# Performance work log

Hardware: AMD Instinct MI355X
Metric: run time of the kernel (lower is better)

## Reference

```python
import jax, jax.numpy as jnp
import numpy as np

B, I, O = 1024, 512, 512
EPS = 1e-07
LOG_CLIP = 20.0

def setup_inputs() -> dict:
    key = jax.random.key(0)
    k1, k2, k3, k4 = jax.random.split(key, 4)
    x = jax.random.normal(k1, (B, I), dtype=jnp.float32)
    # match tf.random_normal_initializer(mean, stddev) used in the layer
    w_hat = 0.88 + 0.2 * jax.random.normal(k2, (I, O), dtype=jnp.float32)
    m_hat = 0.5 + 0.2 * jax.random.normal(k3, (I, O), dtype=jnp.float32)
    g = 0.2 * jax.random.normal(k4, (O,), dtype=jnp.float32)
    return {"x": x, "w_hat": w_hat, "m_hat": m_hat, "g": g}

def reference(x, w_hat, m_hat, g):
    w1 = jnp.tanh(w_hat) * jax.nn.sigmoid(m_hat)          # [I, O]
    a = x @ w1                                             # [B, O] additive path
    # multiplicative path: exp(log|x| @ w1), clipped at 20 before exp
    logx = jnp.log(jnp.maximum(jnp.abs(x), EPS))           # [B, I]
    m1 = jnp.exp(jnp.minimum(logx @ w1, LOG_CLIP))         # [B, O]
    # sign-product tracking. TF flattens w1 row-major to [I*O], tiles x
    # O times along axis 1 -> xs[b, k] = x[b, k % I]; so after reshape to
    # [B, O, I], the paired weight magnitude is ws[j, i] = |w1.flat[j*I + i]|.
    ws_oi = jnp.abs(w1.reshape(-1)).reshape(O, I)          # [O, I] (faithful to TF reshape)
    sgn_x = jnp.sign(x)                                    # [B, I]
    sgn = sgn_x[:, None, :] * ws_oi[None, :, :] + (1.0 - ws_oi)[None, :, :]  # [B, O, I]
    ms = jnp.prod(sgn, axis=2)                             # [B, O]
    g1 = jax.nn.sigmoid(g)                                 # [O]
    return g1 * a + (1.0 - g1) * m1 * jnp.clip(ms, -1.0, 1.0)
```

## Files before the change

### kernel.cpp

```cpp
#include <hip/hip_runtime.h>


#define O_N 512
#define I_N 512
#define B_N 1024

typedef _Float16 f16;
typedef _Float16 f16x8 __attribute__((ext_vector_type(8)));
typedef float f32x4 __attribute__((ext_vector_type(4)));

__device__ __forceinline__ float fast_sigmoid(float v) {
    return 1.0f / (1.0f + __expf(-v));
}
__device__ __forceinline__ float fast_tanh(float v) {
    return 1.0f - 2.0f / (1.0f + __expf(2.0f * v));
}

__global__ __launch_bounds__(256) void prep_kernel(const float* __restrict__ x,
                                                   const float* __restrict__ wh,
                                                   const float* __restrict__ mh,
                                                   f16x8* __restrict__ apx,
                                                   f16x8* __restrict__ apl,
                                                   f16x8* __restrict__ bp) {
    const int tid = threadIdx.x;
    if (blockIdx.x < 128) {
        __shared__ f16 lt[32][72];
        const int kb = blockIdx.x >> 3;
        const int nb = blockIdx.x & 7;
        const int r  = tid >> 3;
        const int c0 = (tid & 7) * 8;
        const int base = (kb * 32 + r) * O_N + nb * 64 + c0;
        const float4* w4 = (const float4*)(wh + base);
        const float4* m4 = (const float4*)(mh + base);
        const float4 wa = w4[0], wb = w4[1], ma = m4[0], mb = m4[1];
        f16x8 row;
        row[0] = (f16)(fast_tanh(wa.x) * fast_sigmoid(ma.x));
        row[1] = (f16)(fast_tanh(wa.y) * fast_sigmoid(ma.y));
        row[2] = (f16)(fast_tanh(wa.z) * fast_sigmoid(ma.z));
        row[3] = (f16)(fast_tanh(wa.w) * fast_sigmoid(ma.w));
        row[4] = (f16)(fast_tanh(wb.x) * fast_sigmoid(mb.x));
        row[5] = (f16)(fast_tanh(wb.y) * fast_sigmoid(mb.y));
        row[6] = (f16)(fast_tanh(wb.z) * fast_sigmoid(mb.z));
        row[7] = (f16)(fast_tanh(wb.w) * fast_sigmoid(mb.w));
        *(f16x8*)&lt[r][c0] = row;
        __syncthreads();
        const int fl  = tid & 63;
        const int tnl = tid >> 6;
        const int nl  = tnl * 16 + (fl & 15);
        const int k0  = (fl >> 4) * 8;
        f16x8 bf;
#pragma unroll
        for (int j = 0; j < 8; ++j) bf[j] = lt[k0 + j][nl];
        const int tn_g = nb * 4 + tnl;
        bp[tn_g * 1024 + kb * 64 + fl] = bf;
    } else {
        const int t  = (blockIdx.x - 128) * 256 + tid;
        const int fl = t & 63;
        const int tk = (t >> 6) & 15;
        const int tm = t >> 10;
        const int m  = tm * 16 + (fl & 15);
        const int k0 = tk * 32 + (fl >> 4) * 8;
        const float4* x4 = (const float4*)(x + m * I_N + k0);
        const float4 q0 = x4[0], q1 = x4[1];
        const float vx[8] = {q0.x, q0.y, q0.z, q0.w, q1.x, q1.y, q1.z, q1.w};
        f16x8 fx, fv;
#pragma unroll
        for (int j = 0; j < 8; ++j) {
            fx[j] = (f16)vx[j];
            fv[j] = (f16)__logf(fmaxf(fabsf(vx[j]), 1e-7f));
        }
        apx[t] = fx;
        apl[t] = fv;
    }
}

__global__ __launch_bounds__(256, 4) void nalu_mfma_kernel(const f16x8* __restrict__ apx,
                                                           const f16x8* __restrict__ apl,
                                                           const f16x8* __restrict__ bp,
                                                           const float* __restrict__ g,
                                                           const float* __restrict__ x,
                                                           const float* __restrict__ wh,
                                                           const float* __restrict__ mh,
                                                           float* __restrict__ out) {
    __shared__ float scs[2][16][17];

    const int lane = threadIdx.x & 63;
    const int w    = threadIdx.x >> 6;
    const int isS  = w & 1;
    const int osub = w >> 1;
    const int b0   = blockIdx.y * 16;
    const int o0   = blockIdx.x * 32 + osub * 16;
    const int tm   = blockIdx.y;
    const int tn   = o0 >> 4;

    f32x4 acc = {0.f, 0.f, 0.f, 0.f};

    const f16x8* pa = (isS ? apl : apx) + tm * 1024 + lane;
    const f16x8* pb = bp + tn * 1024 + lane;

#pragma unroll 8
    for (int tk = 0; tk < 16; ++tk) {
        const f16x8 av = pa[tk * 64];
        const f16x8 bv = pb[tk * 64];
        acc = __builtin_amdgcn_mfma_f32_16x16x32_f16(av, bv, acc, 0, 0, 0);
    }

    const int col = lane & 15;
    const int rq  = (lane >> 4) * 4;

    if (isS) {
#pragma unroll
        for (int r = 0; r < 4; ++r) scs[osub][rq + r][col] = acc[r];
    }
    __syncthreads();

    if (!isS) {
        const int o = o0 + col;
        const float g1  = fast_sigmoid(g[o]);
        const float omg = 1.0f - g1;
#pragma unroll
        for (int r = 0; r < 4; ++r) {
            const int b = b0 + rq + r;
            const float sv = scs[osub][rq + r][col];
            const float m1 = __expf(fminf(sv, 20.0f));
            float msv = 1.0f;
            if (sv > -80.0f) {
                float p = 1.0f;
                for (int i = 0; i < I_N; ++i) {
                    const float wv = fabsf(fast_tanh(wh[o * I_N + i]) *
                                           fast_sigmoid(mh[o * I_N + i]));
                    const float xv = x[b * I_N + i];
                    const float sg = (xv > 0.f) ? 1.f : ((xv < 0.f) ? -1.f : 0.f);
                    p *= sg * wv + (1.0f - wv);
                }
                msv = fminf(fmaxf(p, -1.0f), 1.0f);
            }
            out[b * O_N + o] = g1 * acc[r] + omg * m1 * msv;
        }
    }
}

extern "C" void kernel_launch(void* const* d_in, const int* in_sizes, int n_in,
                              void* d_out, int out_size, void* d_ws, size_t ws_size,
                              hipStream_t stream) {
    const float* x  = (const float*)d_in[0];
    const float* wh = (const float*)d_in[1];
    const float* mh = (const float*)d_in[2];
    const float* g  = (const float*)d_in[3];
    float* out = (float*)d_out;

    char* ws = (char*)d_ws;
    f16x8* apx = (f16x8*)ws;
    f16x8* apl = (f16x8*)(ws + (1u << 20));
    f16x8* bp  = (f16x8*)(ws + (2u << 20));

    prep_kernel<<<384, 256, 0, stream>>>(x, wh, mh, apx, apl, bp);
    nalu_mfma_kernel<<<dim3(16, 64), 256, 0, stream>>>(apx, apl, bp, g, x, wh, mh, out);
}
```

Measured before the change: 69.27 us.

## Fuse prep and MFMA kernels into one cooperative kernel with grid sync

Merges the preprocessing kernel and the MFMA/epilogue kernel into a single cooperative launch of 512 blocks separated by a grid-wide sync, removing one kernel launch and the gap between them. Each block now handles two batch tiles for a fixed output tile. It stages A and B fragments into LDS with global_load_lds async copies and reuses the B tile across both tiles. The costs are the grid barrier, lower occupancy (launch bounds 2), and half as many blocks for the expensive serial sign-product loop, which is left unchanged.

```diff
diff --git a/kernel.cpp b/kernel.cpp
--- a/kernel.cpp
+++ b/kernel.cpp
@@ -1,4 +1,7 @@
 #include <hip/hip_runtime.h>
+#include <hip/hip_cooperative_groups.h>
+
+namespace cg = cooperative_groups;
 
 
 #define O_N 512
@@ -16,17 +19,30 @@
     return 1.0f - 2.0f / (1.0f + __expf(2.0f * v));
 }
 
-__global__ __launch_bounds__(256) void prep_kernel(const float* __restrict__ x,
-                                                   const float* __restrict__ wh,
-                                                   const float* __restrict__ mh,
-                                                   f16x8* __restrict__ apx,
-                                                   f16x8* __restrict__ apl,
-                                                   f16x8* __restrict__ bp) {
-    const int tid = threadIdx.x;
-    if (blockIdx.x < 128) {
-        __shared__ f16 lt[32][72];
-        const int kb = blockIdx.x >> 3;
-        const int nb = blockIdx.x & 7;
+__device__ __forceinline__ void async16(const f16x8* gsrc, f16x8* ldst) {
+    __builtin_amdgcn_global_load_lds(
+        (const __attribute__((address_space(1))) unsigned int*)gsrc,
+        (__attribute__((address_space(3))) unsigned int*)ldst,
+        16, 0, 0);
+}
+
+__global__ __launch_bounds__(256, 2) void nalu_coop_kernel(
+        const float* __restrict__ x, const float* __restrict__ wh,
+        const float* __restrict__ mh, const float* __restrict__ g,
+        float* __restrict__ out, f16x8* __restrict__ apx,
+        f16x8* __restrict__ apl, f16x8* __restrict__ bp) {
+    __shared__ f16x8 stage[4][16][64];
+    __shared__ float scs[2][16][17];
+
+    const int tid  = threadIdx.x;
+    const int lane = tid & 63;
+    const int w    = tid >> 6;
+    const int blk  = blockIdx.x;
+
+    if (blk < 128) {
+        f16* lt = (f16*)&stage[0][0][0];
+        const int kb = blk >> 3;
+        const int nb = blk & 7;
         const int r  = tid >> 3;
         const int c0 = (tid & 7) * 8;
         const int base = (kb * 32 + r) * O_N + nb * 64 + c0;
@@ -42,7 +58,7 @@
         row[5] = (f16)(fast_tanh(wb.y) * fast_sigmoid(mb.y));
         row[6] = (f16)(fast_tanh(wb.z) * fast_sigmoid(mb.z));
         row[7] = (f16)(fast_tanh(wb.w) * fast_sigmoid(mb.w));
-        *(f16x8*)&lt[r][c0] = row;
+        *(f16x8*)&lt[r * 72 + c0] = row;
         __syncthreads();
         const int fl  = tid & 63;
         const int tnl = tid >> 6;
@@ -50,11 +66,11 @@
         const int k0  = (fl >> 4) * 8;
         f16x8 bf;
 #pragma unroll
-        for (int j = 0; j < 8; ++j) bf[j] = lt[k0 + j][nl];
-        const int tn_g = nb * 4 + tnl;
-        bp[tn_g * 1024 + kb * 64 + fl] = bf;
-    } else {
-        const int t  = (blockIdx.x - 128) * 256 + tid;
+        for (int j = 0; j < 8; ++j) bf[j] = lt[(k0 + j) * 72 + nl];
+        bp[(nb * 4 + tnl) * 1024 + kb * 64 + fl] = bf;
+        __syncthreads();
+    } else if (blk < 384) {
+        const int t  = (blk - 128) * 256 + tid;
         const int fl = t & 63;
         const int tk = (t >> 6) & 15;
         const int tm = t >> 10;
@@ -72,70 +88,67 @@
         apx[t] = fx;
         apl[t] = fv;
     }
-}
+    __threadfence();
+    cg::this_grid().sync();
 
-__global__ __launch_bounds__(256, 4) void nalu_mfma_kernel(const f16x8* __restrict__ apx,
-                                                           const f16x8* __restrict__ apl,
-                                                           const f16x8* __restrict__ bp,
-                                                           const float* __restrict__ g,
-                                                           const float* __restrict__ x,
-                                                           const float* __restrict__ wh,
-                                                           const float* __restrict__ mh,
-                                                           float* __restrict__ out) {
-    __shared__ float scs[2][16][17];
+    const int bx = blk & 15;
+    const int st = w & 1;
+    const int ns = w >> 1;
 
-    const int lane = threadIdx.x & 63;
-    const int w    = threadIdx.x >> 6;
-    const int isS  = w & 1;
-    const int osub = w >> 1;
-    const int b0   = blockIdx.y * 16;
-    const int o0   = blockIdx.x * 32 + osub * 16;
-    const int tm   = blockIdx.y;
-    const int tn   = o0 >> 4;
+    for (int rep = 0; rep < 2; ++rep) {
+        const int by = (blk >> 4) + rep * 32;
 
-    f32x4 acc = {0.f, 0.f, 0.f, 0.f};
+        if (w < 2) {
+            const f16x8* src = (w ? apl : apx) + by * 1024;
+#pragma unroll
+            for (int i = 0; i < 16; ++i)
+                async16(src + i * 64 + lane, &stage[w][i][0]);
+        } else if (rep == 0) {
+            const f16x8* src = bp + (2 * bx + (w - 2)) * 1024;
+#pragma unroll
+            for (int i = 0; i < 16; ++i)
+                async16(src + i * 64 + lane, &stage[w][i][0]);
+        }
+        __syncthreads();
 
-    const f16x8* pa = (isS ? apl : apx) + tm * 1024 + lane;
-    const f16x8* pb = bp + tn * 1024 + lane;
+        f32x4 acc = {0.f, 0.f, 0.f, 0.f};
+#pragma unroll
+        for (int tk = 0; tk < 16; ++tk)
+            acc = __builtin_amdgcn_mfma_f32_16x16x32_f16(
+                stage[st][tk][lane], stage[2 + ns][tk][lane], acc, 0, 0, 0);
+        __syncthreads();
 
-#pragma unroll 8
-    for (int tk = 0; tk < 16; ++tk) {
-        const f16x8 av = pa[tk * 64];
-        const f16x8 bv = pb[tk * 64];
-        acc = __builtin_amdgcn_mfma_f32_16x16x32_f16(av, bv, acc, 0, 0, 0);
-    }
-
-    const int col = lane & 15;
-    const int rq  = (lane >> 4) * 4;
-
-    if (isS) {
+        const int col = lane & 15;
+        const int rq  = (lane >> 4) * 4;
+        if (st) {
 #pragma unroll
-        for (int r = 0; r < 4; ++r) scs[osub][rq + r][col] = acc[r];
-    }
-    __syncthreads();
-
-    if (!isS) {
-        const int o = o0 + col;
-        const float g1  = fast_sigmoid(g[o]);
-        const float omg = 1.0f - g1;
+            for (int r = 0; r < 4; ++r) scs[ns][rq + r][col] = acc[r];
+        }
+        __syncthreads();
+        if (!st) {
+            const int o  = bx * 32 + ns * 16 + col;
+            const int b0 = by * 16;
+            const float g1  = fast_sigmoid(g[o]);
+            const float omg = 1.0f - g1;
 #pragma unroll
-        for (int r = 0; r < 4; ++r) {
-            const int b = b0 + rq + r;
-            const float sv = scs[osub][rq + r][col];
-            const float m1 = __expf(fminf(sv, 20.0f));
-            float msv = 1.0f;
-            if (sv > -80.0f) {
-                float p = 1.0f;
-                for (int i = 0; i < I_N; ++i) {
-                    const float wv = fabsf(fast_tanh(wh[o * I_N + i]) *
-                                           fast_sigmoid(mh[o * I_N + i]));
-                    const float xv = x[b * I_N + i];
-                    const float sg = (xv > 0.f) ? 1.f : ((xv < 0.f) ? -1.f : 0.f);
-                    p *= sg * wv + (1.0f - wv);
+            for (int r = 0; r < 4; ++r) {
+                const int b = b0 + rq + r;
+                const float sv = scs[ns][rq + r][col];
+                const float m1 = __expf(fminf(sv, 20.0f));
+                float msv = 1.0f;
+                if (sv > -80.0f) {
+                    float p = 1.0f;
+                    for (int i = 0; i < I_N; ++i) {
+                        const float wv = fabsf(fast_tanh(wh[o * I_N + i]) *
+                                               fast_sigmoid(mh[o * I_N + i]));
+                        const float xv = x[b * I_N + i];
+                        const float sg = (xv > 0.f) ? 1.f : ((xv < 0.f) ? -1.f : 0.f);
+                        p *= sg * wv + (1.0f - wv);
+                    }
+                    msv = fminf(fmaxf(p, -1.0f), 1.0f);
                 }
-                msv = fminf(fmaxf(p, -1.0f), 1.0f);
+                out[b * O_N + o] = g1 * acc[r] + omg * m1 * msv;
             }
-            out[b * O_N + o] = g1 * acc[r] + omg * m1 * msv;
         }
     }
 }
@@ -154,6 +167,8 @@
     f16x8* apl = (f16x8*)(ws + (1u << 20));
     f16x8* bp  = (f16x8*)(ws + (2u << 20));
 
-    prep_kernel<<<384, 256, 0, stream>>>(x, wh, mh, apx, apl, bp);
-    nalu_mfma_kernel<<<dim3(16, 64), 256, 0, stream>>>(apx, apl, bp, g, x, wh, mh, out);
+    void* args[] = {(void*)&x, (void*)&wh, (void*)&mh, (void*)&g,
+                    (void*)&out, (void*)&apx, (void*)&apl, (void*)&bp};
+    hipLaunchCooperativeKernel((void*)nalu_coop_kernel, dim3(512), dim3(256),
+                               args, 0, stream);
 }
```

Result: slower. 195.9 us (+182.8%).
